# Performance work log

Measured on AMD Instinct MI355X. Metric: run time of the kernel, lower is better.

The kernel has to match this reference:

```python
import jax, jax.numpy as jnp
import numpy as np

N = 16384      # total nodes
SEQ = 512      # nodes per graph
NG = 32        # graphs (N = NG*SEQ)
D = 128        # dim_h
H = 8          # heads
E = 262144     # edges
BN_EPS = 1e-5


def _bn(x, g, b):
    # BatchNorm1d, training-mode stats over the node axis (biased var, as torch)
    mu = x.mean(axis=0)
    var = x.var(axis=0)
    return (x - mu) * jax.lax.rsqrt(var + BN_EPS) * g + b


def setup_inputs() -> dict:
    key = jax.random.key(0)
    ks = jax.random.split(key, 24)
    w = lambda k, shp: (jax.random.normal(k, shp, jnp.float32) * 0.05)
    x = jax.random.normal(ks[0], (N, D), jnp.float32)
    # within-graph edges: dst in same graph as src
    src = jax.random.randint(ks[1], (E,), 0, N, dtype=jnp.int32)
    dst = (src // SEQ) * SEQ + jax.random.randint(ks[2], (E,), 0, SEQ, dtype=jnp.int32)
    edge_index = jnp.stack([src, dst])
    edge_attr = jax.random.normal(ks[3], (E, D), jnp.float32)
    return {
        'x': x, 'edge_index': edge_index, 'edge_attr': edge_attr,
        'gin_w1': w(ks[4], (D, D)), 'gin_b1': jnp.zeros((D,), jnp.float32),
        'gin_w2': w(ks[5], (D, D)), 'gin_b2': jnp.zeros((D,), jnp.float32),
        'bn1l_g': jnp.ones((D,), jnp.float32), 'bn1l_b': jnp.zeros((D,), jnp.float32),
        'in_proj_w': w(ks[6], (3 * D, D)), 'in_proj_b': jnp.zeros((3 * D,), jnp.float32),
        'out_proj_w': w(ks[7], (D, D)), 'out_proj_b': jnp.zeros((D,), jnp.float32),
        'bn1a_g': jnp.ones((D,), jnp.float32), 'bn1a_b': jnp.zeros((D,), jnp.float32),
        'ff_w1': w(ks[8], (D, 2 * D)), 'ff_b1': jnp.zeros((2 * D,), jnp.float32),
        'ff_w2': w(ks[9], (2 * D, D)), 'ff_b2': jnp.zeros((D,), jnp.float32),
        'bn2_g': jnp.ones((D,), jnp.float32), 'bn2_b': jnp.zeros((D,), jnp.float32),
    }


def reference(x, edge_index, edge_attr, gin_w1, gin_b1, gin_w2, gin_b2,
              bn1l_g, bn1l_b, in_proj_w, in_proj_b, out_proj_w, out_proj_b,
              bn1a_g, bn1a_b, ff_w1, ff_b1, ff_w2, ff_b2, bn2_g, bn2_b):
    h_in1 = x
    src, dst = edge_index[0], edge_index[1]
    # --- local GINE: aggr_i = sum_{j->i} relu(x_j + e_ji); nn((1+eps)*x + aggr), eps=0
    msg = jax.nn.relu(x[src] + edge_attr)                 # [E, D]
    aggr = jax.ops.segment_sum(msg, dst, num_segments=N)  # [N, D]
    z = x + aggr
    h_local = jax.nn.relu(z @ gin_w1 + gin_b1) @ gin_w2 + gin_b2
    h_local = h_in1 + h_local                # residual (dropout=0)
    h_local = _bn(h_local, bn1l_g, bn1l_b)
    # --- global Transformer attention over dense batch (equal-size graphs => reshape)
    hd = x.reshape(NG, SEQ, D)
    qkv = hd @ in_proj_w.T + in_proj_b       # [NG, SEQ, 3D]
    q, k, v = jnp.split(qkv, 3, axis=-1)
    dh = D // H
    q = q.reshape(NG, SEQ, H, dh)
    k = k.reshape(NG, SEQ, H, dh)
    v = v.reshape(NG, SEQ, H, dh)
    scores = jnp.einsum('bqhd,bkhd->bhqk', q, k) / jnp.sqrt(jnp.float32(dh))
    attn = jax.nn.softmax(scores, axis=-1)
    o = jnp.einsum('bhqk,bkhd->bqhd', attn, v).reshape(NG, SEQ, D)
    h_attn = (o @ out_proj_w.T + out_proj_b).reshape(N, D)
    h_attn = h_in1 + h_attn                  # residual (attn_dropout=0)
    h_attn = _bn(h_attn, bn1a_g, bn1a_b)
    # --- combine + FFN block
    h = h_local + h_attn
    ff = jax.nn.relu(h @ ff_w1 + ff_b1) @ ff_w2 + ff_b2
    h = h + ff
    h = _bn(h, bn2_g, bn2_b)
    return h
```

## Files before the change

kernel.cpp:

```cpp
#include <hip/hip_runtime.h>


#define N_NODES 16384
#define SEQL    512
#define NGRAPH  32
#define DIM     128
#define NHEAD   8
#define DHEAD   16
#define NEDGE   262144

typedef __bf16 bf16;
typedef __bf16 bf16x8 __attribute__((ext_vector_type(8)));
typedef __bf16 bf16x4 __attribute__((ext_vector_type(4)));
typedef float  f32x4  __attribute__((ext_vector_type(4)));

__device__ inline f32x4 mfma16(bf16x8 a, bf16x8 b, f32x4 c) {
  return __builtin_amdgcn_mfma_f32_16x16x32_bf16(a, b, c, 0, 0, 0);
}

__global__ __launch_bounds__(256) void prep_k(
    const float* __restrict__ gw1, const float* __restrict__ gw2,
    const float* __restrict__ ipw, const float* __restrict__ opw,
    const float* __restrict__ fw1, const float* __restrict__ fw2,
    bf16* __restrict__ W, int* __restrict__ cnt, float* __restrict__ stats)
{
  int i = blockIdx.x * 256 + threadIdx.x;
  if (i < 16384) {
    W[i] = (bf16)gw1[(i & 127) * 128 + (i >> 7)];
  } else if (i < 32768) {
    int j = i - 16384;
    W[i] = (bf16)gw2[(j & 127) * 128 + (j >> 7)];
  } else if (i < 81920) {
    W[i] = (bf16)ipw[i - 32768];
  } else if (i < 98304) {
    W[i] = (bf16)opw[i - 81920];
  } else if (i < 131072) {
    int j = i - 98304;
    W[i] = (bf16)fw1[(j & 127) * 256 + (j >> 7)];
  } else if (i < 163840) {
    int j = i - 131072;
    W[i] = (bf16)fw2[(j & 255) * 128 + (j >> 8)];
  } else if (i < 163840 + 16384) {
    cnt[i - 163840] = 0;
  } else if (i < 163840 + 16384 + 768) {
    stats[i - 163840 - 16384] = 0.f;
  }
}

__global__ __launch_bounds__(256) void edge_count_k(const int* __restrict__ ei,
                                                    int* __restrict__ cnt)
{
  int e = blockIdx.x * 256 + threadIdx.x;
  if (e < NEDGE) atomicAdd(&cnt[ei[NEDGE + e]], 1);
}

__global__ __launch_bounds__(1024) void scan_k(const int* __restrict__ cnt,
                                               int* __restrict__ off,
                                               int* __restrict__ cur)
{
  __shared__ int part[1024];
  int t = threadIdx.x;
  int base = t * 16;
  int v[16];
  int s = 0;
#pragma unroll
  for (int j = 0; j < 16; ++j) { v[j] = s; s += cnt[base + j]; }
  part[t] = s;
  __syncthreads();
  for (int d = 1; d < 1024; d <<= 1) {
    int y = (t >= d) ? part[t - d] : 0;
    __syncthreads();
    part[t] += y;
    __syncthreads();
  }
  int bo = (t > 0) ? part[t - 1] : 0;
#pragma unroll
  for (int j = 0; j < 16; ++j) {
    int o = bo + v[j];
    off[base + j] = o;
    cur[base + j] = o;
  }
  if (t == 1023) off[16384] = bo + s;
}

__global__ __launch_bounds__(256) void edge_scatter_k(const int* __restrict__ ei,
                                                      int* __restrict__ cur,
                                                      int2* __restrict__ se)
{
  int e = blockIdx.x * 256 + threadIdx.x;
  if (e < NEDGE) {
    int s = ei[e];
    int d = ei[NEDGE + e];
    int p = atomicAdd(&cur[d], 1);
    se[p] = make_int2(s, e);
  }
}

__global__ __launch_bounds__(256) void aggr_k(
    const float* __restrict__ x, const float* __restrict__ ea,
    const int* __restrict__ off, const int2* __restrict__ se,
    float* __restrict__ z)
{
  int node = blockIdx.x * 4 + (threadIdx.x >> 6);
  int lane = threadIdx.x & 63;
  int c = lane * 2;
  int o0 = off[node], o1 = off[node + 1];
  float a0 = 0.f, a1 = 0.f;
  int j = o0;
  for (; j + 4 <= o1; j += 4) {
    int2 p0 = se[j], p1 = se[j + 1], p2 = se[j + 2], p3 = se[j + 3];
    float2 x0 = *(const float2*)(x + (size_t)p0.x * 128 + c);
    float2 e0 = *(const float2*)(ea + (size_t)p0.y * 128 + c);
    float2 x1 = *(const float2*)(x + (size_t)p1.x * 128 + c);
    float2 e1 = *(const float2*)(ea + (size_t)p1.y * 128 + c);
    float2 x2 = *(const float2*)(x + (size_t)p2.x * 128 + c);
    float2 e2 = *(const float2*)(ea + (size_t)p2.y * 128 + c);
    float2 x3 = *(const float2*)(x + (size_t)p3.x * 128 + c);
    float2 e3 = *(const float2*)(ea + (size_t)p3.y * 128 + c);
    a0 += fmaxf(x0.x + e0.x, 0.f) + fmaxf(x1.x + e1.x, 0.f) +
          fmaxf(x2.x + e2.x, 0.f) + fmaxf(x3.x + e3.x, 0.f);
    a1 += fmaxf(x0.y + e0.y, 0.f) + fmaxf(x1.y + e1.y, 0.f) +
          fmaxf(x2.y + e2.y, 0.f) + fmaxf(x3.y + e3.y, 0.f);
  }
  for (; j < o1; ++j) {
    int2 p = se[j];
    float2 xe = *(const float2*)(x + (size_t)p.x * 128 + c);
    float2 ae = *(const float2*)(ea + (size_t)p.y * 128 + c);
    a0 += fmaxf(xe.x + ae.x, 0.f);
    a1 += fmaxf(xe.y + ae.y, 0.f);
  }
  float2 xn = *(const float2*)(x + (size_t)node * 128 + c);
  *(float2*)(z + (size_t)node * 128 + c) = make_float2(xn.x + a0, xn.y + a1);
}

template <int NCH, int KCH, bool RELU, int RESID, bool STATS, int OUTMODE>
__global__ __launch_bounds__(256) void gemm_k(
    const float* __restrict__ Aptr, const bf16* __restrict__ Wt,
    const float* __restrict__ bias, const float* __restrict__ resid,
    float* __restrict__ outF, bf16* __restrict__ oq, bf16* __restrict__ okk,
    bf16* __restrict__ ov, float* __restrict__ stats)
{
  constexpr int KIN = KCH * 128;
  constexpr int NLD = NCH * 128;
  __shared__ bf16 Alds[32][136];
  __shared__ bf16 Wlds[128][136];
  __shared__ float slds[256];
  int tid = threadIdx.x;
  int wave = tid >> 6, lane = tid & 63, quad = lane >> 4, l16 = lane & 15;
  int rg = wave >> 1, chalf = wave & 1;
  int m0 = blockIdx.x * 32;
  if (STATS) slds[tid] = 0.f;

  for (int nc = 0; nc < NCH; ++nc) {
    f32x4 acc[4];
#pragma unroll
    for (int t = 0; t < 4; ++t) acc[t] = (f32x4){0.f, 0.f, 0.f, 0.f};
    for (int kc = 0; kc < KCH; ++kc) {
      if (!(nc == 0 && kc == 0)) __syncthreads();
      if (nc == 0 || KCH > 1) {
        int r = tid >> 3, c16 = (tid & 7) * 16;
        const float* src = Aptr + (size_t)(m0 + r) * KIN + kc * 128 + c16;
        float4 v0 = *(const float4*)(src);
        float4 v1 = *(const float4*)(src + 4);
        float4 v2 = *(const float4*)(src + 8);
        float4 v3 = *(const float4*)(src + 12);
        *(bf16x8*)&Alds[r][c16] =
            (bf16x8){(bf16)v0.x, (bf16)v0.y, (bf16)v0.z, (bf16)v0.w,
                     (bf16)v1.x, (bf16)v1.y, (bf16)v1.z, (bf16)v1.w};
        *(bf16x8*)&Alds[r][c16 + 8] =
            (bf16x8){(bf16)v2.x, (bf16)v2.y, (bf16)v2.z, (bf16)v2.w,
                     (bf16)v3.x, (bf16)v3.y, (bf16)v3.z, (bf16)v3.w};
      }
      {
        int n = tid >> 1, ch = (tid & 1) * 64;
        const bf16* src = Wt + (size_t)(nc * 128 + n) * KIN + kc * 128 + ch;
        bf16* dst = &Wlds[n][ch];
#pragma unroll
        for (int j = 0; j < 8; ++j)
          *(bf16x8*)(dst + j * 8) = *(const bf16x8*)(src + j * 8);
      }
      __syncthreads();
#pragma unroll
      for (int kt = 0; kt < 4; ++kt) {
        bf16x8 af = *(const bf16x8*)&Alds[rg * 16 + l16][kt * 32 + quad * 8];
#pragma unroll
        for (int nt = 0; nt < 4; ++nt) {
          bf16x8 bfr =
              *(const bf16x8*)&Wlds[chalf * 64 + nt * 16 + l16][kt * 32 + quad * 8];
          acc[nt] = mfma16(af, bfr, acc[nt]);
        }
      }
    }
    int rowb = m0 + rg * 16 + quad * 4;
#pragma unroll
    for (int nt = 0; nt < 4; ++nt) {
      int n = chalf * 64 + nt * 16 + l16;
      int gcol = nc * 128 + n;
      float bv = bias[gcol];
      float vals[4];
#pragma unroll
      for (int r = 0; r < 4; ++r) {
        float v = acc[nt][r] + bv;
        if (RELU) v = fmaxf(v, 0.f);
        if (RESID) v += resid[(size_t)(rowb + r) * 128 + n];
        vals[r] = v;
        if (OUTMODE == 0) {
          outF[(size_t)(rowb + r) * NLD + gcol] = v;
        } else {
          bf16* ob = (nc == 0) ? oq : ((nc == 1) ? okk : ov);
          ob[(size_t)(rowb + r) * 128 + n] = (bf16)v;
        }
      }
      if (STATS) {
        float s = vals[0] + vals[1] + vals[2] + vals[3];
        float q2 = vals[0] * vals[0] + vals[1] * vals[1] +
                   vals[2] * vals[2] + vals[3] * vals[3];
        s += __shfl_xor(s, 16);  s += __shfl_xor(s, 32);
        q2 += __shfl_xor(q2, 16); q2 += __shfl_xor(q2, 32);
        if (quad == 0) {
          atomicAdd(&slds[n * 2], s);
          atomicAdd(&slds[n * 2 + 1], q2);
        }
      }
    }
  }
  if (STATS) {
    __syncthreads();
    if (tid < 128) {
      atomicAdd(&stats[tid], slds[tid * 2]);
      atomicAdd(&stats[128 + tid], slds[tid * 2 + 1]);
    }
  }
}

__global__ __launch_bounds__(256) void attn_k(
    const bf16* __restrict__ qg, const bf16* __restrict__ kg,
    const bf16* __restrict__ vg, float* __restrict__ og)
{
  __shared__ bf16 Klds[512][16];
  __shared__ bf16 Vlds[16][520];
  __shared__ bf16 Plds[4][16][136];
  int b = blockIdx.x;
  int half = b & 1, hh = (b >> 1) & 7, g = b >> 4;
  int tid = threadIdx.x;
  const size_t gbase = (size_t)g * 512 * 128 + hh * 16;
  for (int r = tid; r < 512; r += 256) {
    const bf16* src = kg + gbase + (size_t)r * 128;
    *(bf16x8*)&Klds[r][0] = *(const bf16x8*)src;
    *(bf16x8*)&Klds[r][8] = *(const bf16x8*)(src + 8);
  }
  for (int r = tid; r < 512; r += 256) {
    const bf16* src = vg + gbase + (size_t)r * 128;
#pragma unroll
    for (int d = 0; d < 16; ++d) Vlds[d][r] = src[d];
  }
  __syncthreads();
  int wave = tid >> 6, lane = tid & 63, quad = lane >> 4, l16 = lane & 15;
  const bf16x8 z8 = {};
  for (int it = 0; it < 4; ++it) {
    int qt = half * 16 + it * 4 + wave;
    bf16x8 qf = z8;
    if (quad < 2)
      qf = *(const bf16x8*)(qg + gbase + (size_t)(qt * 16 + l16) * 128 + quad * 8);
    f32x4 S[32];
#pragma unroll
    for (int jt = 0; jt < 32; ++jt) {
      bf16x8 kf = z8;
      if (quad < 2) kf = *(const bf16x8*)&Klds[jt * 16 + l16][quad * 8];
      S[jt] = mfma16(kf, qf, (f32x4){0.f, 0.f, 0.f, 0.f});
    }
    float mx = -1e30f;
#pragma unroll
    for (int jt = 0; jt < 32; ++jt)
#pragma unroll
      for (int r = 0; r < 4; ++r) mx = fmaxf(mx, S[jt][r]);
    mx = fmaxf(mx, __shfl_xor(mx, 16));
    mx = fmaxf(mx, __shfl_xor(mx, 32));
    float sm = 0.f;
#pragma unroll
    for (int jt = 0; jt < 32; ++jt)
#pragma unroll
      for (int r = 0; r < 4; ++r) {
        float e = __expf((S[jt][r] - mx) * 0.25f);
        S[jt][r] = e;
        sm += e;
      }
    sm += __shfl_xor(sm, 16);
    sm += __shfl_xor(sm, 32);
    float rinv = 1.f / sm;
    f32x4 O = (f32x4){0.f, 0.f, 0.f, 0.f};
#pragma unroll
    for (int qd = 0; qd < 4; ++qd) {
#pragma unroll
      for (int jt2 = 0; jt2 < 8; ++jt2)
#pragma unroll
        for (int r = 0; r < 4; ++r)
          Plds[wave][l16][jt2 * 16 + quad * 4 + r] =
              (bf16)(S[qd * 8 + jt2][r] * rinv);
#pragma unroll
      for (int kt = 0; kt < 4; ++kt) {
        bf16x8 pf = *(const bf16x8*)&Plds[wave][l16][kt * 32 + quad * 8];
        bf16x8 vf = *(const bf16x8*)&Vlds[l16][qd * 128 + kt * 32 + quad * 8];
        O = mfma16(vf, pf, O);
      }
    }
    *(float4*)(og + (size_t)(g * 512 + qt * 16 + l16) * 128 + hh * 16 + quad * 4) =
        make_float4(O[0], O[1], O[2], O[3]);
  }
}

__global__ __launch_bounds__(256) void combine_k(
    const float* __restrict__ hl, const float* __restrict__ ha,
    const float* __restrict__ stats,
    const float* __restrict__ g1, const float* __restrict__ b1,
    const float* __restrict__ g2, const float* __restrict__ b2,
    float* __restrict__ h)
{
  __shared__ float sc1[128], sh1[128], sc2[128], sh2[128];
  int tid = threadIdx.x;
  if (tid < 128) {
    const float inv = 1.f / 16384.f;
    float mu = stats[tid] * inv;
    float var = stats[128 + tid] * inv - mu * mu;
    float s = g1[tid] * rsqrtf(var + 1e-5f);
    sc1[tid] = s; sh1[tid] = b1[tid] - mu * s;
    mu = stats[256 + tid] * inv;
    var = stats[384 + tid] * inv - mu * mu;
    s = g2[tid] * rsqrtf(var + 1e-5f);
    sc2[tid] = s; sh2[tid] = b2[tid] - mu * s;
  }
  __syncthreads();
  size_t i = ((size_t)blockIdx.x * 256 + tid) * 4;
  int c = (int)(i & 127);
  float4 a = *(const float4*)(hl + i);
  float4 bb = *(const float4*)(ha + i);
  float4 o;
  o.x = a.x * sc1[c] + sh1[c] + bb.x * sc2[c] + sh2[c];
  o.y = a.y * sc1[c + 1] + sh1[c + 1] + bb.y * sc2[c + 1] + sh2[c + 1];
  o.z = a.z * sc1[c + 2] + sh1[c + 2] + bb.z * sc2[c + 2] + sh2[c + 2];
  o.w = a.w * sc1[c + 3] + sh1[c + 3] + bb.w * sc2[c + 3] + sh2[c + 3];
  *(float4*)(h + i) = o;
}

__global__ __launch_bounds__(256) void apply_k(
    const float* __restrict__ h2, const float* __restrict__ stats,
    const float* __restrict__ g, const float* __restrict__ b,
    float* __restrict__ out)
{
  __shared__ float sc[128], sh[128];
  int tid = threadIdx.x;
  if (tid < 128) {
    const float inv = 1.f / 16384.f;
    float mu = stats[512 + tid] * inv;
    float var = stats[640 + tid] * inv - mu * mu;
    float s = g[tid] * rsqrtf(var + 1e-5f);
    sc[tid] = s; sh[tid] = b[tid] - mu * s;
  }
  __syncthreads();
  size_t i = ((size_t)blockIdx.x * 256 + tid) * 4;
  int c = (int)(i & 127);
  float4 a = *(const float4*)(h2 + i);
  float4 o;
  o.x = a.x * sc[c] + sh[c];
  o.y = a.y * sc[c + 1] + sh[c + 1];
  o.z = a.z * sc[c + 2] + sh[c + 2];
  o.w = a.w * sc[c + 3] + sh[c + 3];
  *(float4*)(out + i) = o;
}

extern "C" void kernel_launch(void* const* d_in, const int* in_sizes, int n_in,
                              void* d_out, int out_size, void* d_ws, size_t ws_size,
                              hipStream_t stream)
{
  (void)in_sizes; (void)n_in; (void)out_size; (void)ws_size;
  const float* x      = (const float*)d_in[0];
  const int*   ei     = (const int*)d_in[1];
  const float* ea     = (const float*)d_in[2];
  const float* gw1    = (const float*)d_in[3];
  const float* gb1    = (const float*)d_in[4];
  const float* gw2    = (const float*)d_in[5];
  const float* gb2    = (const float*)d_in[6];
  const float* bn1l_g = (const float*)d_in[7];
  const float* bn1l_b = (const float*)d_in[8];
  const float* ipw    = (const float*)d_in[9];
  const float* ipb    = (const float*)d_in[10];
  const float* opw    = (const float*)d_in[11];
  const float* opb    = (const float*)d_in[12];
  const float* bn1a_g = (const float*)d_in[13];
  const float* bn1a_b = (const float*)d_in[14];
  const float* fw1    = (const float*)d_in[15];
  const float* fb1    = (const float*)d_in[16];
  const float* fw2    = (const float*)d_in[17];
  const float* fb2    = (const float*)d_in[18];
  const float* bn2_g  = (const float*)d_in[19];
  const float* bn2_b  = (const float*)d_in[20];

  char* ws = (char*)d_ws;
  const size_t KB = 1024, MB = 1048576;
  bf16*  W     = (bf16*)(ws + 0);
  float* stats = (float*)(ws + 320 * KB);
  int*   cnt   = (int*)(ws + 384 * KB);
  int*   off   = (int*)(ws + 448 * KB);
  int*   cur   = (int*)(ws + 576 * KB);
  int2*  se    = (int2*)(ws + 640 * KB);
  float* z   = (float*)(ws + 3 * MB);
  float* hl  = (float*)(ws + 11 * MB);
  bf16*  qb  = (bf16*)(ws + 19 * MB);
  bf16*  kb  = (bf16*)(ws + 23 * MB);
  bf16*  vb  = (bf16*)(ws + 27 * MB);
  float* ob  = (float*)(ws + 31 * MB);
  float* ha  = (float*)(ws + 39 * MB);
  float* hb  = (float*)(ws + 47 * MB);
  float* t1  = (float*)qb;
  float* ff1 = z;
  float* h2  = ob;
  float* out = (float*)d_out;

  prep_k<<<708, 256, 0, stream>>>(gw1, gw2, ipw, opw, fw1, fw2, W, cnt, stats);
  edge_count_k<<<1024, 256, 0, stream>>>(ei, cnt);
  scan_k<<<1, 1024, 0, stream>>>(cnt, off, cur);
  edge_scatter_k<<<1024, 256, 0, stream>>>(ei, cur, se);
  aggr_k<<<4096, 256, 0, stream>>>(x, ea, off, se, z);
  gemm_k<1, 1, true, 0, false, 0><<<512, 256, 0, stream>>>(
      z, W + 0, gb1, nullptr, t1, nullptr, nullptr, nullptr, nullptr);
  gemm_k<1, 1, false, 1, true, 0><<<512, 256, 0, stream>>>(
      t1, W + 16384, gb2, x, hl, nullptr, nullptr, nullptr, stats + 0);
  gemm_k<3, 1, false, 0, false, 1><<<512, 256, 0, stream>>>(
      x, W + 32768, ipb, nullptr, nullptr, qb, kb, vb, nullptr);
  attn_k<<<512, 256, 0, stream>>>(qb, kb, vb, ob);
  gemm_k<1, 1, false, 1, true, 0><<<512, 256, 0, stream>>>(
      ob, W + 81920, opb, x, ha, nullptr, nullptr, nullptr, stats + 256);
  combine_k<<<2048, 256, 0, stream>>>(hl, ha, stats, bn1l_g, bn1l_b, bn1a_g, bn1a_b, hb);
  gemm_k<2, 1, true, 0, false, 0><<<512, 256, 0, stream>>>(
      hb, W + 98304, fb1, nullptr, ff1, nullptr, nullptr, nullptr, nullptr);
  gemm_k<1, 2, false, 1, true, 0><<<512, 256, 0, stream>>>(
      ff1, W + 131072, fb2, hb, h2, nullptr, nullptr, nullptr, stats + 512);
  apply_k<<<2048, 256, 0, stream>>>(h2, stats, bn2_g, bn2_b, out);
}
```

Baseline: 425.1 us.

## Fuse GINE MLP and combine+FFN into single kernels, tidy attention softmax

Merges the two GIN MLP GEMMs into one kernel that keeps the hidden activation in LDS. It also merges the BN combine step with both FFN GEMMs into one kernel that holds the normalized h and the 256-wide hidden in LDS. This removes several fp32 intermediate round trips through global memory and three kernel launches. The attention kernel pads the K tile to avoid bank conflicts, loads V vectorized, splits the max/sum reductions into independent chains, and packs the P stores. The cost is more LDS per block, which may reduce occupancy.

```diff
diff --git a/kernel.cpp b/kernel.cpp
--- a/kernel.cpp
+++ b/kernel.cpp
@@ -16,6 +16,16 @@
 
 __device__ inline f32x4 mfma16(bf16x8 a, bf16x8 b, f32x4 c) {
   return __builtin_amdgcn_mfma_f32_16x16x32_bf16(a, b, c, 0, 0, 0);
+}
+
+__device__ inline void stage_w(const bf16* __restrict__ src0, int stride, int tid,
+                               bf16 (*Wlds)[136]) {
+  int n = tid >> 1, ch = (tid & 1) * 64;
+  const bf16* src = src0 + (size_t)n * stride + ch;
+  bf16* dst = &Wlds[n][ch];
+#pragma unroll
+  for (int j = 0; j < 8; ++j)
+    *(bf16x8*)(dst + j * 8) = *(const bf16x8*)(src + j * 8);
 }
 
 __global__ __launch_bounds__(256) void prep_k(
@@ -133,6 +143,100 @@
   *(float2*)(z + (size_t)node * 128 + c) = make_float2(xn.x + a0, xn.y + a1);
 }
 
+__global__ __launch_bounds__(256) void gine_k(
+    const float* __restrict__ z, const bf16* __restrict__ W,
+    const float* __restrict__ b1, const float* __restrict__ b2,
+    const float* __restrict__ x, float* __restrict__ hl, float* __restrict__ stats)
+{
+  __shared__ bf16 Alds[32][136];
+  __shared__ bf16 Wlds[128][136];
+  __shared__ bf16 Tlds[32][136];
+  __shared__ float slds[256];
+  int tid = threadIdx.x;
+  int wave = tid >> 6, lane = tid & 63, quad = lane >> 4, l16 = lane & 15;
+  int rg = wave >> 1, chalf = wave & 1;
+  int m0 = blockIdx.x * 32;
+  slds[tid] = 0.f;
+  {
+    int r = tid >> 3, c16 = (tid & 7) * 16;
+    const float* src = z + (size_t)(m0 + r) * 128 + c16;
+    float4 v0 = *(const float4*)(src);
+    float4 v1 = *(const float4*)(src + 4);
+    float4 v2 = *(const float4*)(src + 8);
+    float4 v3 = *(const float4*)(src + 12);
+    *(bf16x8*)&Alds[r][c16] =
+        (bf16x8){(bf16)v0.x, (bf16)v0.y, (bf16)v0.z, (bf16)v0.w,
+                 (bf16)v1.x, (bf16)v1.y, (bf16)v1.z, (bf16)v1.w};
+    *(bf16x8*)&Alds[r][c16 + 8] =
+        (bf16x8){(bf16)v2.x, (bf16)v2.y, (bf16)v2.z, (bf16)v2.w,
+                 (bf16)v3.x, (bf16)v3.y, (bf16)v3.z, (bf16)v3.w};
+  }
+  stage_w(W, 128, tid, Wlds);
+  __syncthreads();
+  f32x4 acc[4];
+#pragma unroll
+  for (int t = 0; t < 4; ++t) acc[t] = (f32x4){0.f, 0.f, 0.f, 0.f};
+#pragma unroll
+  for (int kt = 0; kt < 4; ++kt) {
+    bf16x8 af = *(const bf16x8*)&Alds[rg * 16 + l16][kt * 32 + quad * 8];
+#pragma unroll
+    for (int nt = 0; nt < 4; ++nt) {
+      bf16x8 bfr = *(const bf16x8*)&Wlds[chalf * 64 + nt * 16 + l16][kt * 32 + quad * 8];
+      acc[nt] = mfma16(af, bfr, acc[nt]);
+    }
+  }
+  __syncthreads();
+  int rowl = rg * 16 + quad * 4;
+#pragma unroll
+  for (int nt = 0; nt < 4; ++nt) {
+    int n = chalf * 64 + nt * 16 + l16;
+    float bv = b1[n];
+#pragma unroll
+    for (int r = 0; r < 4; ++r)
+      Tlds[rowl + r][n] = (bf16)fmaxf(acc[nt][r] + bv, 0.f);
+  }
+  stage_w(W + 16384, 128, tid, Wlds);
+  __syncthreads();
+#pragma unroll
+  for (int t = 0; t < 4; ++t) acc[t] = (f32x4){0.f, 0.f, 0.f, 0.f};
+#pragma unroll
+  for (int kt = 0; kt < 4; ++kt) {
+    bf16x8 af = *(const bf16x8*)&Tlds[rg * 16 + l16][kt * 32 + quad * 8];
+#pragma unroll
+    for (int nt = 0; nt < 4; ++nt) {
+      bf16x8 bfr = *(const bf16x8*)&Wlds[chalf * 64 + nt * 16 + l16][kt * 32 + quad * 8];
+      acc[nt] = mfma16(af, bfr, acc[nt]);
+    }
+  }
+  int rowb = m0 + rowl;
+#pragma unroll
+  for (int nt = 0; nt < 4; ++nt) {
+    int n = chalf * 64 + nt * 16 + l16;
+    float bv = b2[n];
+    float vals[4];
+#pragma unroll
+    for (int r = 0; r < 4; ++r) {
+      float v = acc[nt][r] + bv + x[(size_t)(rowb + r) * 128 + n];
+      vals[r] = v;
+      hl[(size_t)(rowb + r) * 128 + n] = v;
+    }
+    float s = vals[0] + vals[1] + vals[2] + vals[3];
+    float q2 = vals[0] * vals[0] + vals[1] * vals[1] +
+               vals[2] * vals[2] + vals[3] * vals[3];
+    s += __shfl_xor(s, 16);  s += __shfl_xor(s, 32);
+    q2 += __shfl_xor(q2, 16); q2 += __shfl_xor(q2, 32);
+    if (quad == 0) {
+      atomicAdd(&slds[n * 2], s);
+      atomicAdd(&slds[n * 2 + 1], q2);
+    }
+  }
+  __syncthreads();
+  if (tid < 128) {
+    atomicAdd(&stats[tid], slds[tid * 2]);
+    atomicAdd(&stats[128 + tid], slds[tid * 2 + 1]);
+  }
+}
+
 template <int NCH, int KCH, bool RELU, int RESID, bool STATS, int OUTMODE>
 __global__ __launch_bounds__(256) void gemm_k(
     const float* __restrict__ Aptr, const bf16* __restrict__ Wt,
@@ -171,14 +275,7 @@
             (bf16x8){(bf16)v2.x, (bf16)v2.y, (bf16)v2.z, (bf16)v2.w,
                      (bf16)v3.x, (bf16)v3.y, (bf16)v3.z, (bf16)v3.w};
       }
-      {
-        int n = tid >> 1, ch = (tid & 1) * 64;
-        const bf16* src = Wt + (size_t)(nc * 128 + n) * KIN + kc * 128 + ch;
-        bf16* dst = &Wlds[n][ch];
-#pragma unroll
-        for (int j = 0; j < 8; ++j)
-          *(bf16x8*)(dst + j * 8) = *(const bf16x8*)(src + j * 8);
-      }
+      stage_w(Wt + (size_t)(nc * 128) * KIN + kc * 128, KIN, tid, Wlds);
       __syncthreads();
 #pragma unroll
       for (int kt = 0; kt < 4; ++kt) {
@@ -237,7 +334,7 @@
     const bf16* __restrict__ qg, const bf16* __restrict__ kg,
     const bf16* __restrict__ vg, float* __restrict__ og)
 {
-  __shared__ bf16 Klds[512][16];
+  __shared__ bf16 Klds[512][24];
   __shared__ bf16 Vlds[16][520];
   __shared__ bf16 Plds[4][16][136];
   int b = blockIdx.x;
@@ -251,8 +348,10 @@
   }
   for (int r = tid; r < 512; r += 256) {
     const bf16* src = vg + gbase + (size_t)r * 128;
-#pragma unroll
-    for (int d = 0; d < 16; ++d) Vlds[d][r] = src[d];
+    bf16x8 v0 = *(const bf16x8*)src;
+    bf16x8 v1 = *(const bf16x8*)(src + 8);
+#pragma unroll
+    for (int d = 0; d < 8; ++d) { Vlds[d][r] = v0[d]; Vlds[d + 8][r] = v1[d]; }
   }
   __syncthreads();
   int wave = tid >> 6, lane = tid & 63, quad = lane >> 4, l16 = lane & 15;
@@ -269,22 +368,28 @@
       if (quad < 2) kf = *(const bf16x8*)&Klds[jt * 16 + l16][quad * 8];
       S[jt] = mfma16(kf, qf, (f32x4){0.f, 0.f, 0.f, 0.f});
     }
-    float mx = -1e30f;
-#pragma unroll
-    for (int jt = 0; jt < 32; ++jt)
-#pragma unroll
-      for (int r = 0; r < 4; ++r) mx = fmaxf(mx, S[jt][r]);
+    float m0 = -1e30f, m1 = -1e30f, m2 = -1e30f, m3 = -1e30f;
+#pragma unroll
+    for (int jt = 0; jt < 32; ++jt) {
+      m0 = fmaxf(m0, S[jt][0]);
+      m1 = fmaxf(m1, S[jt][1]);
+      m2 = fmaxf(m2, S[jt][2]);
+      m3 = fmaxf(m3, S[jt][3]);
+    }
+    float mx = fmaxf(fmaxf(m0, m1), fmaxf(m2, m3));
     mx = fmaxf(mx, __shfl_xor(mx, 16));
     mx = fmaxf(mx, __shfl_xor(mx, 32));
-    float sm = 0.f;
-#pragma unroll
-    for (int jt = 0; jt < 32; ++jt)
-#pragma unroll
-      for (int r = 0; r < 4; ++r) {
-        float e = __expf((S[jt][r] - mx) * 0.25f);
-        S[jt][r] = e;
-        sm += e;
-      }
+    float s0 = 0.f, s1 = 0.f, s2 = 0.f, s3 = 0.f;
+#pragma unroll
+    for (int jt = 0; jt < 32; ++jt) {
+      float e0 = __expf((S[jt][0] - mx) * 0.25f);
+      float e1 = __expf((S[jt][1] - mx) * 0.25f);
+      float e2 = __expf((S[jt][2] - mx) * 0.25f);
+      float e3 = __expf((S[jt][3] - mx) * 0.25f);
+      S[jt][0] = e0; S[jt][1] = e1; S[jt][2] = e2; S[jt][3] = e3;
+      s0 += e0; s1 += e1; s2 += e2; s3 += e3;
+    }
+    float sm = (s0 + s1) + (s2 + s3);
     sm += __shfl_xor(sm, 16);
     sm += __shfl_xor(sm, 32);
     float rinv = 1.f / sm;
@@ -292,11 +397,12 @@
 #pragma unroll
     for (int qd = 0; qd < 4; ++qd) {
 #pragma unroll
-      for (int jt2 = 0; jt2 < 8; ++jt2)
-#pragma unroll
-        for (int r = 0; r < 4; ++r)
-          Plds[wave][l16][jt2 * 16 + quad * 4 + r] =
-              (bf16)(S[qd * 8 + jt2][r] * rinv);
+      for (int jt2 = 0; jt2 < 8; ++jt2) {
+        f32x4 sv = S[qd * 8 + jt2];
+        bf16x4 pk = {(bf16)(sv[0] * rinv), (bf16)(sv[1] * rinv),
+                     (bf16)(sv[2] * rinv), (bf16)(sv[3] * rinv)};
+        *(bf16x4*)&Plds[wave][l16][jt2 * 16 + quad * 4] = pk;
+      }
 #pragma unroll
       for (int kt = 0; kt < 4; ++kt) {
         bf16x8 pf = *(const bf16x8*)&Plds[wave][l16][kt * 32 + quad * 8];
@@ -309,37 +415,161 @@
   }
 }
 
-__global__ __launch_bounds__(256) void combine_k(
+__global__ __launch_bounds__(256) void ffn_k(
     const float* __restrict__ hl, const float* __restrict__ ha,
+    const bf16* __restrict__ W1, const bf16* __restrict__ W2,
+    const float* __restrict__ fb1, const float* __restrict__ fb2,
     const float* __restrict__ stats,
-    const float* __restrict__ g1, const float* __restrict__ b1,
-    const float* __restrict__ g2, const float* __restrict__ b2,
-    float* __restrict__ h)
-{
+    const float* __restrict__ g1v, const float* __restrict__ b1v,
+    const float* __restrict__ g2v, const float* __restrict__ b2v,
+    float* __restrict__ h2o, float* __restrict__ so)
+{
+  __shared__ float Hlds[32][132];
+  __shared__ bf16 Ablds[32][136];
+  __shared__ bf16 Wlds[128][136];
+  __shared__ bf16 Tlds[32][264];
   __shared__ float sc1[128], sh1[128], sc2[128], sh2[128];
+  __shared__ float slds[256];
   int tid = threadIdx.x;
+  int wave = tid >> 6, lane = tid & 63, quad = lane >> 4, l16 = lane & 15;
+  int rg = wave >> 1, chalf = wave & 1;
+  int m0 = blockIdx.x * 32;
+  slds[tid] = 0.f;
   if (tid < 128) {
     const float inv = 1.f / 16384.f;
     float mu = stats[tid] * inv;
     float var = stats[128 + tid] * inv - mu * mu;
-    float s = g1[tid] * rsqrtf(var + 1e-5f);
-    sc1[tid] = s; sh1[tid] = b1[tid] - mu * s;
+    float s = g1v[tid] * rsqrtf(var + 1e-5f);
+    sc1[tid] = s; sh1[tid] = b1v[tid] - mu * s;
     mu = stats[256 + tid] * inv;
     var = stats[384 + tid] * inv - mu * mu;
-    s = g2[tid] * rsqrtf(var + 1e-5f);
-    sc2[tid] = s; sh2[tid] = b2[tid] - mu * s;
-  }
-  __syncthreads();
-  size_t i = ((size_t)blockIdx.x * 256 + tid) * 4;
-  int c = (int)(i & 127);
-  float4 a = *(const float4*)(hl + i);
-  float4 bb = *(const float4*)(ha + i);
-  float4 o;
-  o.x = a.x * sc1[c] + sh1[c] + bb.x * sc2[c] + sh2[c];
-  o.y = a.y * sc1[c + 1] + sh1[c + 1] + bb.y * sc2[c + 1] + sh2[c + 1];
-  o.z = a.z * sc1[c + 2] + sh1[c + 2] + bb.z * sc2[c + 2] + sh2[c + 2];
-  o.w = a.w * sc1[c + 3] + sh1[c + 3] + bb.w * sc2[c + 3] + sh2[c + 3];
-  *(float4*)(h + i) = o;
+    s = g2v[tid] * rsqrtf(var + 1e-5f);
+    sc2[tid] = s; sh2[tid] = b2v[tid] - mu * s;
+  }
+  __syncthreads();
+  {
+    int r = tid >> 3, c0 = (tid & 7) * 16;
+    const float* pl = hl + (size_t)(m0 + r) * 128 + c0;
+    const float* pa = ha + (size_t)(m0 + r) * 128 + c0;
+#pragma unroll
+    for (int j = 0; j < 16; j += 8) {
+      float4 a0 = *(const float4*)(pl + j);
+      float4 a1 = *(const float4*)(pl + j + 4);
+      float4 c0v = *(const float4*)(pa + j);
+      float4 c1v = *(const float4*)(pa + j + 4);
+      int c = c0 + j;
+      float h0 = a0.x * sc1[c]     + sh1[c]     + c0v.x * sc2[c]     + sh2[c];
+      float h1 = a0.y * sc1[c + 1] + sh1[c + 1] + c0v.y * sc2[c + 1] + sh2[c + 1];
+      float h2 = a0.z * sc1[c + 2] + sh1[c + 2] + c0v.z * sc2[c + 2] + sh2[c + 2];
+      float h3 = a0.w * sc1[c + 3] + sh1[c + 3] + c0v.w * sc2[c + 3] + sh2[c + 3];
+      float h4 = a1.x * sc1[c + 4] + sh1[c + 4] + c1v.x * sc2[c + 4] + sh2[c + 4];
+      float h5 = a1.y * sc1[c + 5] + sh1[c + 5] + c1v.y * sc2[c + 5] + sh2[c + 5];
+      float h6 = a1.z * sc1[c + 6] + sh1[c + 6] + c1v.z * sc2[c + 6] + sh2[c + 6];
+      float h7 = a1.w * sc1[c + 7] + sh1[c + 7] + c1v.w * sc2[c + 7] + sh2[c + 7];
+      *(float4*)&Hlds[r][c]     = make_float4(h0, h1, h2, h3);
+      *(float4*)&Hlds[r][c + 4] = make_float4(h4, h5, h6, h7);
+      *(bf16x8*)&Ablds[r][c] = (bf16x8){(bf16)h0, (bf16)h1, (bf16)h2, (bf16)h3,
+                                        (bf16)h4, (bf16)h5, (bf16)h6, (bf16)h7};
+    }
+  }
+  stage_w(W1, 128, tid, Wlds);
+  __syncthreads();
+  int rowl = rg * 16 + quad * 4;
+  f32x4 acc[4];
+#pragma unroll
+  for (int t = 0; t < 4; ++t) acc[t] = (f32x4){0.f, 0.f, 0.f, 0.f};
+#pragma unroll
+  for (int kt = 0; kt < 4; ++kt) {
+    bf16x8 af = *(const bf16x8*)&Ablds[rg * 16 + l16][kt * 32 + quad * 8];
+#pragma unroll
+    for (int nt = 0; nt < 4; ++nt) {
+      bf16x8 bfr = *(const bf16x8*)&Wlds[chalf * 64 + nt * 16 + l16][kt * 32 + quad * 8];
+      acc[nt] = mfma16(af, bfr, acc[nt]);
+    }
+  }
+  __syncthreads();
+#pragma unroll
+  for (int nt = 0; nt < 4; ++nt) {
+    int n = chalf * 64 + nt * 16 + l16;
+    float bv = fb1[n];
+#pragma unroll
+    for (int r = 0; r < 4; ++r)
+      Tlds[rowl + r][n] = (bf16)fmaxf(acc[nt][r] + bv, 0.f);
+  }
+  stage_w(W1 + 128 * 128, 128, tid, Wlds);
+  __syncthreads();
+#pragma unroll
+  for (int t = 0; t < 4; ++t) acc[t] = (f32x4){0.f, 0.f, 0.f, 0.f};
+#pragma unroll
+  for (int kt = 0; kt < 4; ++kt) {
+    bf16x8 af = *(const bf16x8*)&Ablds[rg * 16 + l16][kt * 32 + quad * 8];
+#pragma unroll
+    for (int nt = 0; nt < 4; ++nt) {
+      bf16x8 bfr = *(const bf16x8*)&Wlds[chalf * 64 + nt * 16 + l16][kt * 32 + quad * 8];
+      acc[nt] = mfma16(af, bfr, acc[nt]);
+    }
+  }
+  __syncthreads();
+#pragma unroll
+  for (int nt = 0; nt < 4; ++nt) {
+    int n = chalf * 64 + nt * 16 + l16;
+    float bv = fb1[128 + n];
+#pragma unroll
+    for (int r = 0; r < 4; ++r)
+      Tlds[rowl + r][128 + n] = (bf16)fmaxf(acc[nt][r] + bv, 0.f);
+  }
+  stage_w(W2, 256, tid, Wlds);
+  __syncthreads();
+#pragma unroll
+  for (int t = 0; t < 4; ++t) acc[t] = (f32x4){0.f, 0.f, 0.f, 0.f};
+#pragma unroll
+  for (int kt = 0; kt < 4; ++kt) {
+    bf16x8 af = *(const bf16x8*)&Tlds[rg * 16 + l16][kt * 32 + quad * 8];
+#pragma unroll
+    for (int nt = 0; nt < 4; ++nt) {
+      bf16x8 bfr = *(const bf16x8*)&Wlds[chalf * 64 + nt * 16 + l16][kt * 32 + quad * 8];
+      acc[nt] = mfma16(af, bfr, acc[nt]);
+    }
+  }
+  __syncthreads();
+  stage_w(W2 + 128, 256, tid, Wlds);
+  __syncthreads();
+#pragma unroll
+  for (int kt = 0; kt < 4; ++kt) {
+    bf16x8 af = *(const bf16x8*)&Tlds[rg * 16 + l16][128 + kt * 32 + quad * 8];
+#pragma unroll
+    for (int nt = 0; nt < 4; ++nt) {
+      bf16x8 bfr = *(const bf16x8*)&Wlds[chalf * 64 + nt * 16 + l16][kt * 32 + quad * 8];
+      acc[nt] = mfma16(af, bfr, acc[nt]);
+    }
+  }
+  int rowb = m0 + rowl;
+#pragma unroll
+  for (int nt = 0; nt < 4; ++nt) {
+    int n = chalf * 64 + nt * 16 + l16;
+    float bv = fb2[n];
+    float vals[4];
+#pragma unroll
+    for (int r = 0; r < 4; ++r) {
+      float v = acc[nt][r] + bv + Hlds[rowl + r][n];
+      vals[r] = v;
+      h2o[(size_t)(rowb + r) * 128 + n] = v;
+    }
+    float s = vals[0] + vals[1] + vals[2] + vals[3];
+    float q2 = vals[0] * vals[0] + vals[1] * vals[1] +
+               vals[2] * vals[2] + vals[3] * vals[3];
+    s += __shfl_xor(s, 16);  s += __shfl_xor(s, 32);
+    q2 += __shfl_xor(q2, 16); q2 += __shfl_xor(q2, 32);
+    if (quad == 0) {
+      atomicAdd(&slds[n * 2], s);
+      atomicAdd(&slds[n * 2 + 1], q2);
+    }
+  }
+  __syncthreads();
+  if (tid < 128) {
+    atomicAdd(&so[tid], slds[tid * 2]);
+    atomicAdd(&so[128 + tid], slds[tid * 2 + 1]);
+  }
 }
 
 __global__ __launch_bounds__(256) void apply_k(
@@ -410,9 +640,6 @@
   bf16*  vb  = (bf16*)(ws + 27 * MB);
   float* ob  = (float*)(ws + 31 * MB);
   float* ha  = (float*)(ws + 39 * MB);
-  float* hb  = (float*)(ws + 47 * MB);
-  float* t1  = (float*)qb;
-  float* ff1 = z;
   float* h2  = ob;
   float* out = (float*)d_out;
 
@@ -421,19 +648,14 @@
   scan_k<<<1, 1024, 0, stream>>>(cnt, off, cur);
   edge_scatter_k<<<1024, 256, 0, stream>>>(ei, cur, se);
   aggr_k<<<4096, 256, 0, stream>>>(x, ea, off, se, z);
-  gemm_k<1, 1, true, 0, false, 0><<<512, 256, 0, stream>>>(
-      z, W + 0, gb1, nullptr, t1, nullptr, nullptr, nullptr, nullptr);
-  gemm_k<1, 1, false, 1, true, 0><<<512, 256, 0, stream>>>(
-      t1, W + 16384, gb2, x, hl, nullptr, nullptr, nullptr, stats + 0);
+  gine_k<<<512, 256, 0, stream>>>(z, W, gb1, gb2, x, hl, stats + 0);
   gemm_k<3, 1, false, 0, false, 1><<<512, 256, 0, stream>>>(
       x, W + 32768, ipb, nullptr, nullptr, qb, kb, vb, nullptr);
   attn_k<<<512, 256, 0, stream>>>(qb, kb, vb, ob);
   gemm_k<1, 1, false, 1, true, 0><<<512, 256, 0, stream>>>(
       ob, W + 81920, opb, x, ha, nullptr, nullptr, nullptr, stats + 256);
-  combine_k<<<2048, 256, 0, stream>>>(hl, ha, stats, bn1l_g, bn1l_b, bn1a_g, bn1a_b, hb);
-  gemm_k<2, 1, true, 0, false, 0><<<512, 256, 0, stream>>>(
-      hb, W + 98304, fb1, nullptr, ff1, nullptr, nullptr, nullptr, nullptr);
-  gemm_k<1, 2, false, 1, true, 0><<<512, 256, 0, stream>>>(
-      ff1, W + 131072, fb2, hb, h2, nullptr, nullptr, nullptr, stats + 512);
+  ffn_k<<<512, 256, 0, stream>>>(hl, ha, W + 98304, W + 131072, fb1, fb2,
+                                 stats, bn1l_g, bn1l_b, bn1a_g, bn1a_b,
+                                 h2, stats + 512);
   apply_k<<<2048, 256, 0, stream>>>(h2, stats, bn2_g, bn2_b, out);
 }
```

Result: faster. 411.1 us (-3.3%).
